# Performance work log

Hardware: AMD Instinct MI355X
Metric: run time of the kernel (lower is better)

Reference implementation:

```python
import jax, jax.numpy as jnp
import numpy as np

N = 100          # num_objects
H = 128          # decoder_hidden
D = 128          # input_size (== H, required by the module's GRU linears)
REL = 7          # num_relative_features (use_3d=False)
E = N * (N - 1)  # fully-connected, no self loops
B = 32

_mask = ~np.eye(N, dtype=bool)
_SEND_NP, _RECV_NP = np.where(_mask)  # torch.where(~eye): rows=send, cols=recv
SEND = jnp.asarray(_SEND_NP, dtype=jnp.int32)
RECV = jnp.asarray(_RECV_NP, dtype=jnp.int32)


def setup_inputs() -> dict:
    key = jax.random.key(0)
    ks = jax.random.split(key, 34)
    def w(k, shape, scale=0.05):
        return jax.random.normal(k, shape, dtype=jnp.float32) * scale
    inp = {
        "inputs": jax.random.normal(ks[0], (B, N, D), jnp.float32),
        "edge_attr": jax.random.normal(ks[1], (B, E, REL + D), jnp.float32),
        "hidden": jax.random.normal(ks[2], (B, N, H), jnp.float32),
        # msg_mlp: Linear(2H,H) Tanh Linear(H,H) Tanh
        "msg_w1": w(ks[3], (2 * H, H)), "msg_b1": w(ks[4], (H,)),
        "msg_w2": w(ks[5], (H, H)),     "msg_b2": w(ks[6], (H,)),
        # present_msg_mlp: Linear(REL+D,H) ReLU Linear(H,H) ReLU
        "pm_w1": w(ks[7], (REL + D, H)), "pm_b1": w(ks[8], (H,)),
        "pm_w2": w(ks[9], (H, H)),       "pm_b2": w(ks[10], (H,)),
        # res_mlp: Linear(D,H) ReLU Linear(H,H) ReLU
        "res_w1": w(ks[11], (D, H)), "res_b1": w(ks[12], (H,)),
        "res_w2": w(ks[13], (H, H)), "res_b2": w(ks[14], (H,)),
        # GRU-style gates
        "ir_w": w(ks[15], (H, H)), "ir_b": w(ks[16], (H,)),
        "ii_w": w(ks[17], (H, H)), "ii_b": w(ks[18], (H,)),
        "in_w": w(ks[19], (H, H)), "in_b": w(ks[20], (H,)),
        "hr_w": w(ks[21], (H, H)),
        "hi_w": w(ks[22], (H, H)),
        "hh_w": w(ks[23], (H, H)),
        # out_mlp: Linear(H,H) ReLU Linear(H,H) ReLU Linear(H,D)
        "out_w1": w(ks[24], (H, H)), "out_b1": w(ks[25], (H,)),
        "out_w2": w(ks[26], (H, H)), "out_b2": w(ks[27], (H,)),
        "out_w3": w(ks[28], (H, D)), "out_b3": w(ks[29], (D,)),
    }
    return inp


def _scatter_mean(msgs, recv, num_nodes):
    # msgs: [B, E, H] -> [B, N, H], mean over incoming edges per node
    counts = jnp.zeros((num_nodes,), msgs.dtype).at[recv].add(1.0)
    summed = jnp.zeros((msgs.shape[0], num_nodes, msgs.shape[-1]), msgs.dtype)
    summed = summed.at[:, recv].add(msgs)
    return summed / counts[None, :, None]


def reference(inputs, edge_attr, hidden,
              msg_w1, msg_b1, msg_w2, msg_b2,
              pm_w1, pm_b1, pm_w2, pm_b2,
              res_w1, res_b1, res_w2, res_b2,
              ir_w, ir_b, ii_w, ii_b, in_w, in_b,
              hr_w, hi_w, hh_w,
              out_w1, out_b1, out_w2, out_b2, out_w3, out_b3):
    # gather hidden states along edges (dropout is identity: p=0 / eval)
    hm = jnp.concatenate([hidden[:, RECV], hidden[:, SEND]], axis=-1)  # [B,E,2H]
    hm = jnp.tanh(jnp.tanh(hm @ msg_w1 + msg_b1) @ msg_w2 + msg_b2)
    hidden_node = _scatter_mean(hm, RECV, N)                           # [B,N,H]

    pm = jax.nn.relu(jax.nn.relu(edge_attr @ pm_w1 + pm_b1) @ pm_w2 + pm_b2)
    present_node = _scatter_mean(pm, RECV, N)
    present_node = present_node + jax.nn.relu(
        jax.nn.relu(inputs @ res_w1 + res_b1) @ res_w2 + res_b2)

    r = jax.nn.sigmoid(present_node @ ir_w + ir_b + hidden_node @ hr_w)
    i = jax.nn.sigmoid(present_node @ ii_w + ii_b + hidden_node @ hi_w)
    n = jnp.tanh(present_node @ in_w + in_b + r * (hidden_node @ hh_w))
    hidden_new = (1.0 - i) * n + i * hidden

    pred = jax.nn.relu(hidden_new @ out_w1 + out_b1)
    pred = jax.nn.relu(pred @ out_w2 + out_b2)
    pred = pred @ out_w3 + out_b3
    return pred, hidden_new
```

## Files before the change

kernel.cpp:

```cpp
#include <hip/hip_runtime.h>

typedef unsigned short u16;
typedef unsigned int   u32;
typedef __attribute__((ext_vector_type(8))) short bf8;
typedef __attribute__((ext_vector_type(4))) float f4;

#define DF __device__ __forceinline__

DF float bf2f(u16 h){ u32 u = ((u32)h) << 16; float f; __builtin_memcpy(&f, &u, 4); return f; }
DF u16 f2bf(float f){ u32 u; __builtin_memcpy(&u, &f, 4); u = (u + 0x7FFFu + ((u >> 16) & 1u)) >> 16; return (u16)u; }
DF float fexp2(float x){ return __builtin_amdgcn_exp2f(x); }
DF float frcp (float x){ return __builtin_amdgcn_rcpf(x); }
DF float tanhF(float x){ float e = fexp2(2.8853900817779268f * x); return 1.0f - 2.0f * frcp(e + 1.0f); }
DF float sigF (float x){ return frcp(1.0f + fexp2(-1.4426950408889634f * x)); }
DF float4 ld4u(const float* p){ float4 v; __builtin_memcpy(&v, p, 16); return v; }
DF u32 cvtpk(float lo, float hi){ u32 r; asm("v_cvt_pk_bf16_f32 %0, %1, %2" : "=v"(r) : "v"(lo), "v"(hi)); return r; }

DF const bf8* fragp(const u16* packed, int w, int nt, int ks, int lane){
  return reinterpret_cast<const bf8*>(packed + (((w * 32 + nt * 4 + ks) * 64 + lane) * 8));
}
DF const bf8* fragp_pm1(const u16* packed, int nt, int ks, int lane){
  return reinterpret_cast<const bf8*>(packed + (((512 + nt * 5 + ks) * 64 + lane) * 8));
}

struct WPtrs { const float* p[16]; };

__global__ __launch_bounds__(256) void k_pack(WPtrs wp, u16* __restrict__ packed){
  int bi = blockIdx.x;
  int lane = threadIdx.x & 63, warp = threadIdx.x >> 6;
  if(bi == 16){
    const float* __restrict__ src = wp.p[14];
    u16* __restrict__ dst = packed + 512 * 64 * 8;
    for(int i = warp; i < 40; i += 4){
      int nt = i / 5, ks = i - nt * 5;
      int col = nt * 16 + (lane & 15);
      int kb  = ks * 32 + (lane >> 4) * 8;
      u16* o = dst + (i * 64 + lane) * 8;
      for(int j = 0; j < 8; j++){
        int row = kb + j;
        o[j] = (row < 135) ? f2bf(src[row * 128 + col]) : (u16)0;
      }
    }
    return;
  }
  const float* __restrict__ src = wp.p[bi];
  u16* __restrict__ dst = packed + bi * 32 * 64 * 8;
  for(int i = warp; i < 32; i += 4){
    int nt = i >> 2, ks = i & 3;
    int col = nt * 16 + (lane & 15);
    int kb  = ks * 32 + (lane >> 4) * 8;
    u16* o = dst + (i * 64 + lane) * 8;
    for(int j = 0; j < 8; j++) o[j] = f2bf(src[(kb + j) * 128 + col]);
  }
}

__global__ __launch_bounds__(512) void k_node_pre(
    const float* __restrict__ hidden, const float* __restrict__ inputs,
    const u16* __restrict__ packed,
    const float* __restrict__ res_b1, const float* __restrict__ res_b2,
    float* __restrict__ Ptop, float* __restrict__ Pbot, float* __restrict__ res2)
{
  __shared__ __align__(16) u16 hid[64 * 136];
  __shared__ __align__(16) u16 inp[64 * 136];
  __shared__ __align__(16) u16 t1s[64 * 136];
  int row0 = blockIdx.x * 64;
  int t = threadIdx.x, lane = t & 63, w = t >> 6;
  int lrow = lane & 15, lk = lane >> 4;
  for(int i = t; i < 64 * 128; i += 512){
    int rr = i >> 7, cc = i & 127;
    hid[rr * 136 + cc] = f2bf(hidden[(row0 + rr) * 128 + cc]);
    inp[rr * 136 + cc] = f2bf(inputs[(row0 + rr) * 128 + cc]);
  }
  int col = w * 16 + lrow;
  float rb1 = res_b1[col], rb2 = res_b2[col];
  __syncthreads();
  {
    bf8 f0[4], f1[4], f5[4];
    #pragma unroll
    for(int k = 0; k < 4; k++){
      f0[k] = *fragp(packed, 0, w, k, lane);
      f1[k] = *fragp(packed, 1, w, k, lane);
      f5[k] = *fragp(packed, 5, w, k, lane);
    }
    #pragma unroll
    for(int m = 0; m < 4; m++){
      bf8 a[4], a2[4];
      #pragma unroll
      for(int k = 0; k < 4; k++){
        a[k]  = *reinterpret_cast<const bf8*>(&hid[(m * 16 + lrow) * 136 + k * 32 + lk * 8]);
        a2[k] = *reinterpret_cast<const bf8*>(&inp[(m * 16 + lrow) * 136 + k * 32 + lk * 8]);
      }
      f4 c0 = {0.f,0.f,0.f,0.f}, c1 = {0.f,0.f,0.f,0.f}, c2 = {0.f,0.f,0.f,0.f};
      #pragma unroll
      for(int k = 0; k < 4; k++){
        c0 = __builtin_amdgcn_mfma_f32_16x16x32_bf16(a[k],  f0[k], c0, 0, 0, 0);
        c1 = __builtin_amdgcn_mfma_f32_16x16x32_bf16(a[k],  f1[k], c1, 0, 0, 0);
        c2 = __builtin_amdgcn_mfma_f32_16x16x32_bf16(a2[k], f5[k], c2, 0, 0, 0);
      }
      #pragma unroll
      for(int q = 0; q < 4; q++){
        int gr = row0 + m * 16 + lk * 4 + q;
        Ptop[gr * 128 + col] = c0[q];
        Pbot[gr * 128 + col] = c1[q];
        float v = c2[q] + rb1; v = v > 0.f ? v : 0.f;
        t1s[(m * 16 + lk * 4 + q) * 136 + col] = f2bf(v);
      }
    }
  }
  __syncthreads();
  {
    bf8 f6[4];
    #pragma unroll
    for(int k = 0; k < 4; k++) f6[k] = *fragp(packed, 6, w, k, lane);
    #pragma unroll
    for(int m = 0; m < 4; m++){
      bf8 a3[4];
      #pragma unroll
      for(int k = 0; k < 4; k++)
        a3[k] = *reinterpret_cast<const bf8*>(&t1s[(m * 16 + lrow) * 136 + k * 32 + lk * 8]);
      f4 c = {0.f,0.f,0.f,0.f};
      #pragma unroll
      for(int k = 0; k < 4; k++)
        c = __builtin_amdgcn_mfma_f32_16x16x32_bf16(a3[k], f6[k], c, 0, 0, 0);
      #pragma unroll
      for(int q = 0; q < 4; q++){
        float v = c[q] + rb2; v = v > 0.f ? v : 0.f;
        res2[(row0 + m * 16 + lk * 4 + q) * 128 + col] = v;
      }
    }
  }
}

__global__ __launch_bounds__(512, 4) void k_edge(
    const float* __restrict__ EA,
    const float* __restrict__ Ptop, const float* __restrict__ Pbot,
    const float* __restrict__ msg_b1, const float* __restrict__ msg_b2,
    const float* __restrict__ pm_b1, const float* __restrict__ pm_b2,
    const u16* __restrict__ packed,
    float* __restrict__ hnode, float* __restrict__ pnode)
{
  __shared__ __align__(16) u16 bufA[112 * 128];
  __shared__ __align__(16) u16 tail[112 * 8];
  char* bb = (char*)bufA;
  char* tb = (char*)tail;
  int blk = blockIdx.x;
  int b = blk / 100, r = blk - b * 100;
  int t = threadIdx.x, lane = t & 63, w = t >> 6;
  int lrow = lane & 15, lk = lane >> 4;

  {
    for(int i = t; i < 99 * 16; i += 512){
      int row = i >> 4, g = i & 15;
      int s = row + (row >= r ? 1 : 0);
      int e = s * 99 + (r < s ? r : r - 1);
      const float* rp = EA + ((size_t)(b * 9900 + e)) * 135 + g * 8;
      float4 v0 = ld4u(rp), v1 = ld4u(rp + 4);
      u32 pk[4] = {cvtpk(v0.x, v0.y), cvtpk(v0.z, v0.w), cvtpk(v1.x, v1.y), cvtpk(v1.z, v1.w)};
      *reinterpret_cast<uint4*>(bb + row * 256 + ((g ^ (row & 7)) << 4)) = *reinterpret_cast<const uint4*>(pk);
    }
    for(int row = t; row < 99; row += 512){
      int s = row + (row >= r ? 1 : 0);
      int e = s * 99 + (r < s ? r : r - 1);
      const float* rp = EA + ((size_t)(b * 9900 + e)) * 135 + 128;
      float4 v0 = ld4u(rp);
      u32 pk[4] = {cvtpk(v0.x, v0.y), cvtpk(v0.z, v0.w), cvtpk(rp[4], rp[5]), cvtpk(rp[6], 0.f)};
      *reinterpret_cast<uint4*>(tb + row * 16) = *reinterpret_cast<const uint4*>(pk);
    }
    bf8 w1[5];
    #pragma unroll
    for(int k = 0; k < 5; k++) w1[k] = *fragp_pm1(packed, w, k, lane);
    asm volatile("" : "+v"(w1[0]), "+v"(w1[1]), "+v"(w1[2]), "+v"(w1[3]), "+v"(w1[4]));
    float b1 = pm_b1[w * 16 + lrow];
    __syncthreads();

    f4 cA[4];
    #pragma unroll
    for(int m = 0; m < 4; m++){
      int arow = m * 16 + lrow, sw = arow & 7;
      bf8 a[4];
      #pragma unroll
      for(int k = 0; k < 4; k++)
        a[k] = *reinterpret_cast<const bf8*>(bb + arow * 256 + (((k * 4 + lk) ^ sw) << 4));
      bf8 a4 = {0,0,0,0,0,0,0,0};
      if(lk == 0) a4 = *reinterpret_cast<const bf8*>(tb + arow * 16);
      f4 c = {0.f,0.f,0.f,0.f};
      #pragma unroll
      for(int k = 0; k < 4; k++)
        c = __builtin_amdgcn_mfma_f32_16x16x32_bf16(a[k], w1[k], c, 0, 0, 0);
      c = __builtin_amdgcn_mfma_f32_16x16x32_bf16(a4, w1[4], c, 0, 0, 0);
      cA[m] = c;
    }
    __syncthreads();

    #pragma unroll
    for(int m = 0; m < 4; m++){
      #pragma unroll
      for(int qp = 0; qp < 2; qp++){
        float v0 = cA[m][2*qp]   + b1; v0 = v0 > 0.f ? v0 : 0.f;
        float u0 = cA[m][2*qp+1] + b1; u0 = u0 > 0.f ? u0 : 0.f;
        u32 p0 = cvtpk(v0, u0);
        int row0_ = m * 16 + lk * 4 + 2 * qp;
        int sw0 = (row0_ & 7) << 4, sw1 = ((row0_ + 1) & 7) << 4;
        *reinterpret_cast<u16*>(bb + row0_ * 256       + (((w * 16 + lrow) * 2) ^ sw0)) = (u16)p0;
        *reinterpret_cast<u16*>(bb + (row0_ + 1) * 256 + (((w * 16 + lrow) * 2) ^ sw1)) = (u16)(p0 >> 16);
      }
    }
    f4 cB[3];
    #pragma unroll
    for(int m = 0; m < 3; m++){
      int arow = (m + 4) * 16 + lrow, sw = arow & 7;
      bf8 a[4];
      #pragma unroll
      for(int k = 0; k < 4; k++)
        a[k] = *reinterpret_cast<const bf8*>(bb + arow * 256 + (((k * 4 + lk) ^ sw) << 4));
      bf8 a4 = {0,0,0,0,0,0,0,0};
      if(lk == 0) a4 = *reinterpret_cast<const bf8*>(tb + arow * 16);
      f4 c = {0.f,0.f,0.f,0.f};
      #pragma unroll
      for(int k = 0; k < 4; k++)
        c = __builtin_amdgcn_mfma_f32_16x16x32_bf16(a[k], w1[k], c, 0, 0, 0);
      c = __builtin_amdgcn_mfma_f32_16x16x32_bf16(a4, w1[4], c, 0, 0, 0);
      cB[m] = c;
    }
    __syncthreads();

    #pragma unroll
    for(int m = 0; m < 3; m++){
      #pragma unroll
      for(int qp = 0; qp < 2; qp++){
        float v0 = cB[m][2*qp]   + b1; v0 = v0 > 0.f ? v0 : 0.f;
        float u0 = cB[m][2*qp+1] + b1; u0 = u0 > 0.f ? u0 : 0.f;
        u32 p0 = cvtpk(v0, u0);
        int row0_ = (m + 4) * 16 + lk * 4 + 2 * qp;
        int sw0 = (row0_ & 7) << 4, sw1 = ((row0_ + 1) & 7) << 4;
        *reinterpret_cast<u16*>(bb + row0_ * 256       + (((w * 16 + lrow) * 2) ^ sw0)) = (u16)p0;
        *reinterpret_cast<u16*>(bb + (row0_ + 1) * 256 + (((w * 16 + lrow) * 2) ^ sw1)) = (u16)(p0 >> 16);
      }
    }
    __syncthreads();

    bf8 w2[4];
    #pragma unroll
    for(int k = 0; k < 4; k++) w2[k] = *fragp(packed, 15, w, k, lane);
    float b2 = pm_b2[w * 16 + lrow];
    float acc = 0.f;
    #pragma unroll
    for(int m = 0; m < 7; m++){
      int arow = m * 16 + lrow, sw = arow & 7;
      bf8 a[4];
      #pragma unroll
      for(int k = 0; k < 4; k++)
        a[k] = *reinterpret_cast<const bf8*>(bb + arow * 256 + (((k * 4 + lk) ^ sw) << 4));
      f4 c = {0.f,0.f,0.f,0.f};
      #pragma unroll
      for(int k = 0; k < 4; k++)
        c = __builtin_amdgcn_mfma_f32_16x16x32_bf16(a[k], w2[k], c, 0, 0, 0);
      #pragma unroll
      for(int q = 0; q < 4; q++){
        int rr = m * 16 + lk * 4 + q;
        if(rr < 99){ float v = c[q] + b2; acc += (v > 0.f ? v : 0.f); }
      }
    }
    acc += __shfl_xor(acc, 16); acc += __shfl_xor(acc, 32);
    if(lane < 16) pnode[((size_t)b * 100 + r) * 128 + w * 16 + lane] = acc * (1.0f / 99.0f);
  }
  __syncthreads();

  {
    bf8 w2[4];
    #pragma unroll
    for(int k = 0; k < 4; k++) w2[k] = *fragp(packed, 13, w, k, lane);
    float b2 = msg_b2[w * 16 + lrow];
    int c4 = t & 31;
    float4 pt = *reinterpret_cast<const float4*>(Ptop + ((size_t)b * 100 + r) * 128 + c4 * 4);
    float4 mb = *reinterpret_cast<const float4*>(msg_b1 + c4 * 4);
    pt.x += mb.x; pt.y += mb.y; pt.z += mb.z; pt.w += mb.w;
    for(int row = t >> 5; row < 99; row += 16){
      int s = row + (row >= r ? 1 : 0);
      float4 v = *reinterpret_cast<const float4*>(Pbot + ((size_t)b * 100 + s) * 128 + c4 * 4);
      u32 pk[2] = {cvtpk(tanhF(pt.x + v.x), tanhF(pt.y + v.y)),
                   cvtpk(tanhF(pt.z + v.z), tanhF(pt.w + v.w))};
      *reinterpret_cast<uint2*>(bb + row * 256 + ((8 * c4) ^ ((row & 7) << 4))) = *reinterpret_cast<const uint2*>(pk);
    }
    __syncthreads();
    float acc = 0.f;
    #pragma unroll
    for(int m = 0; m < 7; m++){
      int arow = m * 16 + lrow, sw = arow & 7;
      bf8 a[4];
      #pragma unroll
      for(int k = 0; k < 4; k++)
        a[k] = *reinterpret_cast<const bf8*>(bb + arow * 256 + (((k * 4 + lk) ^ sw) << 4));
      f4 c = {0.f,0.f,0.f,0.f};
      #pragma unroll
      for(int k = 0; k < 4; k++)
        c = __builtin_amdgcn_mfma_f32_16x16x32_bf16(a[k], w2[k], c, 0, 0, 0);
      #pragma unroll
      for(int q = 0; q < 4; q++){
        int rr = m * 16 + lk * 4 + q;
        if(rr < 99) acc += tanhF(c[q] + b2);
      }
    }
    acc += __shfl_xor(acc, 16); acc += __shfl_xor(acc, 32);
    if(lane < 16) hnode[((size_t)b * 100 + r) * 128 + w * 16 + lane] = acc * (1.0f / 99.0f);
  }
}

__global__ __launch_bounds__(512) void k_final(
    const float* __restrict__ hnode, const float* __restrict__ pnode,
    const float* __restrict__ res2, const float* __restrict__ hidden,
    const u16* __restrict__ packed,
    const float* __restrict__ ir_b, const float* __restrict__ ii_b, const float* __restrict__ in_b,
    const float* __restrict__ ob1, const float* __restrict__ ob2, const float* __restrict__ ob3,
    float* __restrict__ out_pred, float* __restrict__ out_hid)
{
  __shared__ __align__(16) u16 hn[64 * 136];
  __shared__ __align__(16) u16 pr[64 * 136];
  __shared__ __align__(16) u16 hw[64 * 136];
  int row0 = blockIdx.x * 64;
  int t = threadIdx.x, lane = t & 63, w = t >> 6;
  int lrow = lane & 15, lk = lane >> 4;
  for(int i = t; i < 64 * 128; i += 512){
    int rr = i >> 7, cc = i & 127;
    hn[rr * 136 + cc] = f2bf(hnode[(row0 + rr) * 128 + cc]);
    pr[rr * 136 + cc] = f2bf(pnode[(row0 + rr) * 128 + cc] + res2[(row0 + rr) * 128 + cc]);
  }
  int col = w * 16 + lrow;
  float bir = ir_b[col], bii = ii_b[col], bin = in_b[col];
  __syncthreads();
  #pragma unroll
  for(int m = 0; m < 4; m++){
    bf8 a[4], p[4];
    #pragma unroll
    for(int k = 0; k < 4; k++){
      a[k] = *reinterpret_cast<const bf8*>(&hn[(m * 16 + lrow) * 136 + k * 32 + lk * 8]);
      p[k] = *reinterpret_cast<const bf8*>(&pr[(m * 16 + lrow) * 136 + k * 32 + lk * 8]);
    }
    f4 cR = {0.f,0.f,0.f,0.f}, cI = {0.f,0.f,0.f,0.f}, cN = {0.f,0.f,0.f,0.f};
    f4 dR = {0.f,0.f,0.f,0.f}, dI = {0.f,0.f,0.f,0.f}, dN = {0.f,0.f,0.f,0.f};
    #pragma unroll
    for(int k = 0; k < 4; k++){
      cR = __builtin_amdgcn_mfma_f32_16x16x32_bf16(a[k], *fragp(packed, 2, w, k, lane), cR, 0, 0, 0);
      cI = __builtin_amdgcn_mfma_f32_16x16x32_bf16(a[k], *fragp(packed, 3, w, k, lane), cI, 0, 0, 0);
      cN = __builtin_amdgcn_mfma_f32_16x16x32_bf16(a[k], *fragp(packed, 4, w, k, lane), cN, 0, 0, 0);
      dR = __builtin_amdgcn_mfma_f32_16x16x32_bf16(p[k], *fragp(packed, 7, w, k, lane), dR, 0, 0, 0);
      dI = __builtin_amdgcn_mfma_f32_16x16x32_bf16(p[k], *fragp(packed, 8, w, k, lane), dI, 0, 0, 0);
      dN = __builtin_amdgcn_mfma_f32_16x16x32_bf16(p[k], *fragp(packed, 9, w, k, lane), dN, 0, 0, 0);
    }
    #pragma unroll
    for(int q = 0; q < 4; q++){
      int gr = row0 + m * 16 + lk * 4 + q;
      float rv = sigF(dR[q] + bir + cR[q]);
      float iv = sigF(dI[q] + bii + cI[q]);
      float nv = tanhF(dN[q] + bin + rv * cN[q]);
      float hold = hidden[gr * 128 + col];
      float hnew = (1.f - iv) * nv + iv * hold;
      out_hid[gr * 128 + col] = hnew;
      hw[(m * 16 + lk * 4 + q) * 136 + col] = f2bf(hnew);
    }
  }
  __syncthreads();
  {
    bf8 m10[4];
    #pragma unroll
    for(int k = 0; k < 4; k++) m10[k] = *fragp(packed, 10, w, k, lane);
    float bb = ob1[col];
    #pragma unroll
    for(int m = 0; m < 4; m++){
      f4 c = {0.f,0.f,0.f,0.f};
      #pragma unroll
      for(int k = 0; k < 4; k++){
        bf8 a = *reinterpret_cast<const bf8*>(&hw[(m * 16 + lrow) * 136 + k * 32 + lk * 8]);
        c = __builtin_amdgcn_mfma_f32_16x16x32_bf16(a, m10[k], c, 0, 0, 0);
      }
      #pragma unroll
      for(int q = 0; q < 4; q++){
        float v = c[q] + bb; v = v > 0.f ? v : 0.f;
        hn[(m * 16 + lk * 4 + q) * 136 + col] = f2bf(v);
      }
    }
  }
  __syncthreads();
  {
    bf8 m11[4];
    #pragma unroll
    for(int k = 0; k < 4; k++) m11[k] = *fragp(packed, 11, w, k, lane);
    float bb = ob2[col];
    #pragma unroll
    for(int m = 0; m < 4; m++){
      f4 c = {0.f,0.f,0.f,0.f};
      #pragma unroll
      for(int k = 0; k < 4; k++){
        bf8 a = *reinterpret_cast<const bf8*>(&hn[(m * 16 + lrow) * 136 + k * 32 + lk * 8]);
        c = __builtin_amdgcn_mfma_f32_16x16x32_bf16(a, m11[k], c, 0, 0, 0);
      }
      #pragma unroll
      for(int q = 0; q < 4; q++){
        float v = c[q] + bb; v = v > 0.f ? v : 0.f;
        pr[(m * 16 + lk * 4 + q) * 136 + col] = f2bf(v);
      }
    }
  }
  __syncthreads();
  {
    bf8 m12[4];
    #pragma unroll
    for(int k = 0; k < 4; k++) m12[k] = *fragp(packed, 12, w, k, lane);
    float bb = ob3[col];
    #pragma unroll
    for(int m = 0; m < 4; m++){
      f4 c = {0.f,0.f,0.f,0.f};
      #pragma unroll
      for(int k = 0; k < 4; k++){
        bf8 a = *reinterpret_cast<const bf8*>(&pr[(m * 16 + lrow) * 136 + k * 32 + lk * 8]);
        c = __builtin_amdgcn_mfma_f32_16x16x32_bf16(a, m12[k], c, 0, 0, 0);
      }
      #pragma unroll
      for(int q = 0; q < 4; q++)
        out_pred[(row0 + m * 16 + lk * 4 + q) * 128 + col] = c[q] + bb;
    }
  }
}

extern "C" void kernel_launch(void* const* d_in, const int* in_sizes, int n_in,
                              void* d_out, int out_size, void* d_ws, size_t ws_size,
                              hipStream_t stream)
{
  const float* inputs = (const float*)d_in[0];
  const float* edge   = (const float*)d_in[1];
  const float* hidden = (const float*)d_in[2];
  const float* msg_w1 = (const float*)d_in[3];
  const float* msg_b1 = (const float*)d_in[4];
  const float* msg_w2 = (const float*)d_in[5];
  const float* msg_b2 = (const float*)d_in[6];
  const float* pm_w1  = (const float*)d_in[7];
  const float* pm_b1  = (const float*)d_in[8];
  const float* pm_w2  = (const float*)d_in[9];
  const float* pm_b2  = (const float*)d_in[10];
  const float* res_w1 = (const float*)d_in[11];
  const float* res_b1 = (const float*)d_in[12];
  const float* res_w2 = (const float*)d_in[13];
  const float* res_b2 = (const float*)d_in[14];
  const float* ir_w = (const float*)d_in[15]; const float* ir_b = (const float*)d_in[16];
  const float* ii_w = (const float*)d_in[17]; const float* ii_b = (const float*)d_in[18];
  const float* in_w = (const float*)d_in[19]; const float* in_b = (const float*)d_in[20];
  const float* hr_w = (const float*)d_in[21];
  const float* hi_w = (const float*)d_in[22];
  const float* hh_w = (const float*)d_in[23];
  const float* out_w1 = (const float*)d_in[24]; const float* out_b1 = (const float*)d_in[25];
  const float* out_w2 = (const float*)d_in[26]; const float* out_b2 = (const float*)d_in[27];
  const float* out_w3 = (const float*)d_in[28]; const float* out_b3 = (const float*)d_in[29];

  char* ws = (char*)d_ws;
  u16*   packed = (u16*)ws;
  float* Ptop   = (float*)(ws + (1 << 20));
  float* Pbot   = (float*)(ws + (1 << 20) + 1 * 1638400);
  float* res2   = (float*)(ws + (1 << 20) + 2 * 1638400);
  float* hnode  = (float*)(ws + (1 << 20) + 3 * 1638400);
  float* pnode  = (float*)(ws + (1 << 20) + 4 * 1638400);

  WPtrs wp;
  wp.p[0]  = msg_w1;
  wp.p[1]  = msg_w1 + 128 * 128;
  wp.p[2]  = hr_w;  wp.p[3]  = hi_w;  wp.p[4]  = hh_w;
  wp.p[5]  = res_w1; wp.p[6] = res_w2;
  wp.p[7]  = ir_w;  wp.p[8]  = ii_w;  wp.p[9]  = in_w;
  wp.p[10] = out_w1; wp.p[11] = out_w2; wp.p[12] = out_w3;
  wp.p[13] = msg_w2; wp.p[14] = pm_w1; wp.p[15] = pm_w2;

  k_pack<<<17, 256, 0, stream>>>(wp, packed);
  k_node_pre<<<50, 512, 0, stream>>>(hidden, inputs, packed, res_b1, res_b2, Ptop, Pbot, res2);
  k_edge<<<3200, 512, 0, stream>>>(edge, Ptop, Pbot, msg_b1, msg_b2, pm_b1, pm_b2,
                                   packed, hnode, pnode);
  float* outp = (float*)d_out;
  k_final<<<50, 512, 0, stream>>>(hnode, pnode, res2, hidden, packed,
                                  ir_b, ii_b, in_b, out_b1, out_b2, out_b3,
                                  outp, outp + 32 * 100 * 128);
}
```

Baseline: 129.6 us.

## Pad edge LDS rows, split MFMA accumulators, pack stores, hoist GRU weights

In k_edge, the XOR-swizzled 256-byte LDS rows become padded 272-byte rows, and the layer-1 results are packed in pairs via a lane shuffle into 32-bit LDS stores instead of 16-bit ones. Each MFMA chain now uses two interleaved accumulators to shorten the dependent chain. Occupancy hint drops from 4 to 3 blocks, and w2 fragments are pinned in registers. In k_final, the six gate weight fragment sets are loaded once before the row loop rather than per iteration, which raises register pressure.

```diff
diff --git a/kernel.cpp b/kernel.cpp
--- a/kernel.cpp
+++ b/kernel.cpp
@@ -131,7 +131,7 @@
   }
 }
 
-__global__ __launch_bounds__(512, 4) void k_edge(
+__global__ __launch_bounds__(512, 3) void k_edge(
     const float* __restrict__ EA,
     const float* __restrict__ Ptop, const float* __restrict__ Pbot,
     const float* __restrict__ msg_b1, const float* __restrict__ msg_b2,
@@ -139,7 +139,7 @@
     const u16* __restrict__ packed,
     float* __restrict__ hnode, float* __restrict__ pnode)
 {
-  __shared__ __align__(16) u16 bufA[112 * 128];
+  __shared__ __align__(16) u16 bufA[112 * 136];
   __shared__ __align__(16) u16 tail[112 * 8];
   char* bb = (char*)bufA;
   char* tb = (char*)tail;
@@ -156,7 +156,7 @@
       const float* rp = EA + ((size_t)(b * 9900 + e)) * 135 + g * 8;
       float4 v0 = ld4u(rp), v1 = ld4u(rp + 4);
       u32 pk[4] = {cvtpk(v0.x, v0.y), cvtpk(v0.z, v0.w), cvtpk(v1.x, v1.y), cvtpk(v1.z, v1.w)};
-      *reinterpret_cast<uint4*>(bb + row * 256 + ((g ^ (row & 7)) << 4)) = *reinterpret_cast<const uint4*>(pk);
+      *reinterpret_cast<uint4*>(bb + row * 272 + g * 16) = *reinterpret_cast<const uint4*>(pk);
     }
     for(int row = t; row < 99; row += 512){
       int s = row + (row >= r ? 1 : 0);
@@ -176,65 +176,67 @@
     f4 cA[4];
     #pragma unroll
     for(int m = 0; m < 4; m++){
-      int arow = m * 16 + lrow, sw = arow & 7;
+      int arow = m * 16 + lrow;
       bf8 a[4];
       #pragma unroll
       for(int k = 0; k < 4; k++)
-        a[k] = *reinterpret_cast<const bf8*>(bb + arow * 256 + (((k * 4 + lk) ^ sw) << 4));
+        a[k] = *reinterpret_cast<const bf8*>(bb + arow * 272 + k * 64 + lk * 16);
       bf8 a4 = {0,0,0,0,0,0,0,0};
       if(lk == 0) a4 = *reinterpret_cast<const bf8*>(tb + arow * 16);
-      f4 c = {0.f,0.f,0.f,0.f};
-      #pragma unroll
-      for(int k = 0; k < 4; k++)
-        c = __builtin_amdgcn_mfma_f32_16x16x32_bf16(a[k], w1[k], c, 0, 0, 0);
-      c = __builtin_amdgcn_mfma_f32_16x16x32_bf16(a4, w1[4], c, 0, 0, 0);
-      cA[m] = c;
+      f4 ce = {0.f,0.f,0.f,0.f}, co = {0.f,0.f,0.f,0.f};
+      ce = __builtin_amdgcn_mfma_f32_16x16x32_bf16(a[0], w1[0], ce, 0, 0, 0);
+      co = __builtin_amdgcn_mfma_f32_16x16x32_bf16(a[1], w1[1], co, 0, 0, 0);
+      ce = __builtin_amdgcn_mfma_f32_16x16x32_bf16(a[2], w1[2], ce, 0, 0, 0);
+      co = __builtin_amdgcn_mfma_f32_16x16x32_bf16(a[3], w1[3], co, 0, 0, 0);
+      ce = __builtin_amdgcn_mfma_f32_16x16x32_bf16(a4,   w1[4], ce, 0, 0, 0);
+      cA[m] = ce + co;
     }
     __syncthreads();
 
     #pragma unroll
     for(int m = 0; m < 4; m++){
       #pragma unroll
-      for(int qp = 0; qp < 2; qp++){
-        float v0 = cA[m][2*qp]   + b1; v0 = v0 > 0.f ? v0 : 0.f;
-        float u0 = cA[m][2*qp+1] + b1; u0 = u0 > 0.f ? u0 : 0.f;
-        u32 p0 = cvtpk(v0, u0);
-        int row0_ = m * 16 + lk * 4 + 2 * qp;
-        int sw0 = (row0_ & 7) << 4, sw1 = ((row0_ + 1) & 7) << 4;
-        *reinterpret_cast<u16*>(bb + row0_ * 256       + (((w * 16 + lrow) * 2) ^ sw0)) = (u16)p0;
-        *reinterpret_cast<u16*>(bb + (row0_ + 1) * 256 + (((w * 16 + lrow) * 2) ^ sw1)) = (u16)(p0 >> 16);
+      for(int q = 0; q < 4; q++){
+        float v = cA[m][q] + b1; v = v > 0.f ? v : 0.f;
+        float o = __shfl_xor(v, 1);
+        u32 p = cvtpk(v, o);
+        if(!(lrow & 1)){
+          int row_ = m * 16 + lk * 4 + q;
+          *reinterpret_cast<u32*>(bb + row_ * 272 + (w * 16 + lrow) * 2) = p;
+        }
       }
     }
     f4 cB[3];
     #pragma unroll
     for(int m = 0; m < 3; m++){
-      int arow = (m + 4) * 16 + lrow, sw = arow & 7;
+      int arow = (m + 4) * 16 + lrow;
       bf8 a[4];
       #pragma unroll
       for(int k = 0; k < 4; k++)
-        a[k] = *reinterpret_cast<const bf8*>(bb + arow * 256 + (((k * 4 + lk) ^ sw) << 4));
+        a[k] = *reinterpret_cast<const bf8*>(bb + arow * 272 + k * 64 + lk * 16);
       bf8 a4 = {0,0,0,0,0,0,0,0};
       if(lk == 0) a4 = *reinterpret_cast<const bf8*>(tb + arow * 16);
-      f4 c = {0.f,0.f,0.f,0.f};
-      #pragma unroll
-      for(int k = 0; k < 4; k++)
-        c = __builtin_amdgcn_mfma_f32_16x16x32_bf16(a[k], w1[k], c, 0, 0, 0);
-      c = __builtin_amdgcn_mfma_f32_16x16x32_bf16(a4, w1[4], c, 0, 0, 0);
-      cB[m] = c;
+      f4 ce = {0.f,0.f,0.f,0.f}, co = {0.f,0.f,0.f,0.f};
+      ce = __builtin_amdgcn_mfma_f32_16x16x32_bf16(a[0], w1[0], ce, 0, 0, 0);
+      co = __builtin_amdgcn_mfma_f32_16x16x32_bf16(a[1], w1[1], co, 0, 0, 0);
+      ce = __builtin_amdgcn_mfma_f32_16x16x32_bf16(a[2], w1[2], ce, 0, 0, 0);
+      co = __builtin_amdgcn_mfma_f32_16x16x32_bf16(a[3], w1[3], co, 0, 0, 0);
+      ce = __builtin_amdgcn_mfma_f32_16x16x32_bf16(a4,   w1[4], ce, 0, 0, 0);
+      cB[m] = ce + co;
     }
     __syncthreads();
 
     #pragma unroll
     for(int m = 0; m < 3; m++){
       #pragma unroll
-      for(int qp = 0; qp < 2; qp++){
-        float v0 = cB[m][2*qp]   + b1; v0 = v0 > 0.f ? v0 : 0.f;
-        float u0 = cB[m][2*qp+1] + b1; u0 = u0 > 0.f ? u0 : 0.f;
-        u32 p0 = cvtpk(v0, u0);
-        int row0_ = (m + 4) * 16 + lk * 4 + 2 * qp;
-        int sw0 = (row0_ & 7) << 4, sw1 = ((row0_ + 1) & 7) << 4;
-        *reinterpret_cast<u16*>(bb + row0_ * 256       + (((w * 16 + lrow) * 2) ^ sw0)) = (u16)p0;
-        *reinterpret_cast<u16*>(bb + (row0_ + 1) * 256 + (((w * 16 + lrow) * 2) ^ sw1)) = (u16)(p0 >> 16);
+      for(int q = 0; q < 4; q++){
+        float v = cB[m][q] + b1; v = v > 0.f ? v : 0.f;
+        float o = __shfl_xor(v, 1);
+        u32 p = cvtpk(v, o);
+        if(!(lrow & 1)){
+          int row_ = (m + 4) * 16 + lk * 4 + q;
+          *reinterpret_cast<u32*>(bb + row_ * 272 + (w * 16 + lrow) * 2) = p;
+        }
       }
     }
     __syncthreads();
@@ -242,23 +244,25 @@
     bf8 w2[4];
     #pragma unroll
     for(int k = 0; k < 4; k++) w2[k] = *fragp(packed, 15, w, k, lane);
+    asm volatile("" : "+v"(w2[0]), "+v"(w2[1]), "+v"(w2[2]), "+v"(w2[3]));
     float b2 = pm_b2[w * 16 + lrow];
     float acc = 0.f;
     #pragma unroll
     for(int m = 0; m < 7; m++){
-      int arow = m * 16 + lrow, sw = arow & 7;
+      int arow = m * 16 + lrow;
       bf8 a[4];
       #pragma unroll
       for(int k = 0; k < 4; k++)
-        a[k] = *reinterpret_cast<const bf8*>(bb + arow * 256 + (((k * 4 + lk) ^ sw) << 4));
-      f4 c = {0.f,0.f,0.f,0.f};
-      #pragma unroll
-      for(int k = 0; k < 4; k++)
-        c = __builtin_amdgcn_mfma_f32_16x16x32_bf16(a[k], w2[k], c, 0, 0, 0);
+        a[k] = *reinterpret_cast<const bf8*>(bb + arow * 272 + k * 64 + lk * 16);
+      f4 ce = {0.f,0.f,0.f,0.f}, co = {0.f,0.f,0.f,0.f};
+      ce = __builtin_amdgcn_mfma_f32_16x16x32_bf16(a[0], w2[0], ce, 0, 0, 0);
+      co = __builtin_amdgcn_mfma_f32_16x16x32_bf16(a[1], w2[1], co, 0, 0, 0);
+      ce = __builtin_amdgcn_mfma_f32_16x16x32_bf16(a[2], w2[2], ce, 0, 0, 0);
+      co = __builtin_amdgcn_mfma_f32_16x16x32_bf16(a[3], w2[3], co, 0, 0, 0);
       #pragma unroll
       for(int q = 0; q < 4; q++){
         int rr = m * 16 + lk * 4 + q;
-        if(rr < 99){ float v = c[q] + b2; acc += (v > 0.f ? v : 0.f); }
+        if(rr < 99){ float v = ce[q] + co[q] + b2; acc += (v > 0.f ? v : 0.f); }
       }
     }
     acc += __shfl_xor(acc, 16); acc += __shfl_xor(acc, 32);
@@ -270,6 +274,7 @@
     bf8 w2[4];
     #pragma unroll
     for(int k = 0; k < 4; k++) w2[k] = *fragp(packed, 13, w, k, lane);
+    asm volatile("" : "+v"(w2[0]), "+v"(w2[1]), "+v"(w2[2]), "+v"(w2[3]));
     float b2 = msg_b2[w * 16 + lrow];
     int c4 = t & 31;
     float4 pt = *reinterpret_cast<const float4*>(Ptop + ((size_t)b * 100 + r) * 128 + c4 * 4);
@@ -280,25 +285,26 @@
       float4 v = *reinterpret_cast<const float4*>(Pbot + ((size_t)b * 100 + s) * 128 + c4 * 4);
       u32 pk[2] = {cvtpk(tanhF(pt.x + v.x), tanhF(pt.y + v.y)),
                    cvtpk(tanhF(pt.z + v.z), tanhF(pt.w + v.w))};
-      *reinterpret_cast<uint2*>(bb + row * 256 + ((8 * c4) ^ ((row & 7) << 4))) = *reinterpret_cast<const uint2*>(pk);
+      *reinterpret_cast<uint2*>(bb + row * 272 + 8 * c4) = *reinterpret_cast<const uint2*>(pk);
     }
     __syncthreads();
     float acc = 0.f;
     #pragma unroll
     for(int m = 0; m < 7; m++){
-      int arow = m * 16 + lrow, sw = arow & 7;
+      int arow = m * 16 + lrow;
       bf8 a[4];
       #pragma unroll
       for(int k = 0; k < 4; k++)
-        a[k] = *reinterpret_cast<const bf8*>(bb + arow * 256 + (((k * 4 + lk) ^ sw) << 4));
-      f4 c = {0.f,0.f,0.f,0.f};
-      #pragma unroll
-      for(int k = 0; k < 4; k++)
-        c = __builtin_amdgcn_mfma_f32_16x16x32_bf16(a[k], w2[k], c, 0, 0, 0);
+        a[k] = *reinterpret_cast<const bf8*>(bb + arow * 272 + k * 64 + lk * 16);
+      f4 ce = {0.f,0.f,0.f,0.f}, co = {0.f,0.f,0.f,0.f};
+      ce = __builtin_amdgcn_mfma_f32_16x16x32_bf16(a[0], w2[0], ce, 0, 0, 0);
+      co = __builtin_amdgcn_mfma_f32_16x16x32_bf16(a[1], w2[1], co, 0, 0, 0);
+      ce = __builtin_amdgcn_mfma_f32_16x16x32_bf16(a[2], w2[2], ce, 0, 0, 0);
+      co = __builtin_amdgcn_mfma_f32_16x16x32_bf16(a[3], w2[3], co, 0, 0, 0);
       #pragma unroll
       for(int q = 0; q < 4; q++){
         int rr = m * 16 + lk * 4 + q;
-        if(rr < 99) acc += tanhF(c[q] + b2);
+        if(rr < 99) acc += tanhF(ce[q] + co[q] + b2);
       }
     }
     acc += __shfl_xor(acc, 16); acc += __shfl_xor(acc, 32);
@@ -326,6 +332,16 @@
     pr[rr * 136 + cc] = f2bf(pnode[(row0 + rr) * 128 + cc] + res2[(row0 + rr) * 128 + cc]);
   }
   int col = w * 16 + lrow;
+  bf8 mhr[4], mhi[4], mhh[4], mir[4], mii[4], min_[4];
+  #pragma unroll
+  for(int k = 0; k < 4; k++){
+    mhr[k]  = *fragp(packed, 2, w, k, lane);
+    mhi[k]  = *fragp(packed, 3, w, k, lane);
+    mhh[k]  = *fragp(packed, 4, w, k, lane);
+    mir[k]  = *fragp(packed, 7, w, k, lane);
+    mii[k]  = *fragp(packed, 8, w, k, lane);
+    min_[k] = *fragp(packed, 9, w, k, lane);
+  }
   float bir = ir_b[col], bii = ii_b[col], bin = in_b[col];
   __syncthreads();
   #pragma unroll
@@ -340,12 +356,12 @@
     f4 dR = {0.f,0.f,0.f,0.f}, dI = {0.f,0.f,0.f,0.f}, dN = {0.f,0.f,0.f,0.f};
     #pragma unroll
     for(int k = 0; k < 4; k++){
-      cR = __builtin_amdgcn_mfma_f32_16x16x32_bf16(a[k], *fragp(packed, 2, w, k, lane), cR, 0, 0, 0);
-      cI = __builtin_amdgcn_mfma_f32_16x16x32_bf16(a[k], *fragp(packed, 3, w, k, lane), cI, 0, 0, 0);
-      cN = __builtin_amdgcn_mfma_f32_16x16x32_bf16(a[k], *fragp(packed, 4, w, k, lane), cN, 0, 0, 0);
-      dR = __builtin_amdgcn_mfma_f32_16x16x32_bf16(p[k], *fragp(packed, 7, w, k, lane), dR, 0, 0, 0);
-      dI = __builtin_amdgcn_mfma_f32_16x16x32_bf16(p[k], *fragp(packed, 8, w, k, lane), dI, 0, 0, 0);
-      dN = __builtin_amdgcn_mfma_f32_16x16x32_bf16(p[k], *fragp(packed, 9, w, k, lane), dN, 0, 0, 0);
+      cR = __builtin_amdgcn_mfma_f32_16x16x32_bf16(a[k], mhr[k],  cR, 0, 0, 0);
+      cI = __builtin_amdgcn_mfma_f32_16x16x32_bf16(a[k], mhi[k],  cI, 0, 0, 0);
+      cN = __builtin_amdgcn_mfma_f32_16x16x32_bf16(a[k], mhh[k],  cN, 0, 0, 0);
+      dR = __builtin_amdgcn_mfma_f32_16x16x32_bf16(p[k], mir[k],  dR, 0, 0, 0);
+      dI = __builtin_amdgcn_mfma_f32_16x16x32_bf16(p[k], mii[k],  dI, 0, 0, 0);
+      dN = __builtin_amdgcn_mfma_f32_16x16x32_bf16(p[k], min_[k], dN, 0, 0, 0);
     }
     #pragma unroll
     for(int q = 0; q < 4; q++){
```

New measurement: 135.0 us. 4.1% more time.
